# Kernel optimization log

Measured on AMD Instinct MI355X. Metric: run time of the kernel, lower is better.

## Reference

```python
import jax, jax.numpy as jnp
import numpy as np

REG_COEF = 25.0


def setup_inputs() -> dict:
    key = jax.random.key(0)
    k1, k2, k3, k4 = jax.random.split(key, 4)
    B, C, N, RES = 32, 4, 16384, 32
    y_pred = jax.random.normal(k1, (B, C, 4), dtype=jnp.float32)
    points = jax.random.uniform(k2, (B, N, 3), dtype=jnp.float32)  # unit cube
    voxel_grid = jax.random.uniform(k3, (B, RES, RES, RES), dtype=jnp.float32)
    voxel_grid_cp = jax.random.uniform(k4, (B, RES, RES, RES, 3), dtype=jnp.float32)
    return {"y_pred": y_pred, "points": points, "voxel_grid": voxel_grid,
            "voxel_grid_cp": voxel_grid_cp}


def _sym_loss(y_pred, points, voxel_grid, voxel_grid_cp):
    B, C, _ = y_pred.shape
    res = voxel_grid_cp.shape[1]
    normals = y_pred[:, :, 0:3]                       # [B,C,3]
    n_hat = normals / jnp.linalg.norm(normals, axis=-1, keepdims=True)
    d = y_pred[:, :, 3]                               # [B,C]

    # --- regularization loss: ||N N^T - I||_F per batch item, then mean ---
    gram = jnp.einsum('bcd,bed->bce', n_hat, n_hat) - jnp.eye(C, dtype=y_pred.dtype)
    reg_loss = jnp.linalg.norm(gram, axis=(1, 2))     # [B]

    # --- reflexion loss: reflect points across each plane, gather closest points ---
    # signed distance to plane: points . n_hat + d  -> [B,C,N]
    dist = jnp.einsum('bnd,bcd->bcn', points, n_hat) + d[:, :, None]
    reflected = points[:, None, :, :] - 2.0 * dist[..., None] * n_hat[:, :, None, :]  # [B,C,N,3]

    vox = jnp.clip(jnp.floor(reflected * res), 0, res - 1).astype(jnp.int32)  # [B,C,N,3]
    b_idx = jnp.arange(B)[:, None, None]
    cp = voxel_grid_cp[b_idx, vox[..., 0], vox[..., 1], vox[..., 2]]          # [B,C,N,3]

    per_plane = jnp.linalg.norm(reflected - cp, axis=-1).mean(axis=-1)        # [B,C]
    reflexion_loss = per_plane.sum()

    return jnp.reshape(reflexion_loss + REG_COEF * reg_loss.mean(), (1,))


def reference(y_pred, points, voxel_grid, voxel_grid_cp):
    return _sym_loss(y_pred, points, voxel_grid, voxel_grid_cp)
```

## Files before the change

### kernel.cpp

```cpp
#include <hip/hip_runtime.h>
#include <math.h>

#define B_    32
#define C_    4
#define N_    16384
#define RES_  32

#define CHUNKS 64
#define TPB    256

__global__ __launch_bounds__(TPB) void sym_main(
    const float* __restrict__ y_pred,
    const float* __restrict__ points,
    const float* __restrict__ cp,
    float* __restrict__ partials)
{
  const int id   = blockIdx.x;
  const int xcd  = id & 7;
  const int slot = id >> 3;
  const int b     = xcd + 8 * (slot & 3);
  const int chunk = slot >> 2;

  const float* yp = y_pred + b * (C_ * 4);
  float nx[C_], ny[C_], nz[C_], dd[C_];
#pragma unroll
  for (int c = 0; c < C_; ++c) {
    float ax = yp[c * 4 + 0];
    float ay = yp[c * 4 + 1];
    float az = yp[c * 4 + 2];
    float inv = 1.0f / sqrtf(ax * ax + ay * ay + az * az);
    nx[c] = ax * inv;
    ny[c] = ay * inv;
    nz[c] = az * inv;
    dd[c] = yp[c * 4 + 3];
  }

  const float* pb  = points + (size_t)b * (N_ * 3);
  const float* cpb = cp + (size_t)b * (RES_ * RES_ * RES_ * 3);

  const int p = chunk * TPB + threadIdx.x;
  const float px = pb[p * 3 + 0];
  const float py = pb[p * 3 + 1];
  const float pz = pb[p * 3 + 2];

  float rx[C_], ry[C_], rz[C_];
  int lin[C_];
#pragma unroll
  for (int c = 0; c < C_; ++c) {
    float dist = px * nx[c] + py * ny[c] + pz * nz[c] + dd[c];
    float t2 = 2.0f * dist;
    float x = px - t2 * nx[c];
    float y = py - t2 * ny[c];
    float z = pz - t2 * nz[c];
    rx[c] = x; ry[c] = y; rz[c] = z;
    int vx = (int)fminf(fmaxf(floorf(x * (float)RES_), 0.0f), (float)(RES_ - 1));
    int vy = (int)fminf(fmaxf(floorf(y * (float)RES_), 0.0f), (float)(RES_ - 1));
    int vz = (int)fminf(fmaxf(floorf(z * (float)RES_), 0.0f), (float)(RES_ - 1));
    lin[c] = ((vx * RES_ + vy) * RES_ + vz) * 3;
  }

  float cx[C_], cy[C_], cz[C_];
#pragma unroll
  for (int c = 0; c < C_; ++c) {
    cx[c] = cpb[lin[c] + 0];
    cy[c] = cpb[lin[c] + 1];
    cz[c] = cpb[lin[c] + 2];
  }

  float a0 = 0.0f, a1 = 0.0f;
#pragma unroll
  for (int c = 0; c < C_; c += 2) {
    float dx0 = rx[c+0] - cx[c+0], dy0 = ry[c+0] - cy[c+0], dz0 = rz[c+0] - cz[c+0];
    float dx1 = rx[c+1] - cx[c+1], dy1 = ry[c+1] - cy[c+1], dz1 = rz[c+1] - cz[c+1];
    a0 += sqrtf(dx0 * dx0 + dy0 * dy0 + dz0 * dz0);
    a1 += sqrtf(dx1 * dx1 + dy1 * dy1 + dz1 * dz1);
  }
  float acc = a0 + a1;

#pragma unroll
  for (int off = 32; off > 0; off >>= 1)
    acc += __shfl_down(acc, off, 64);

  __shared__ float sred[TPB / 64];
  const int lane = threadIdx.x & 63;
  const int wave = threadIdx.x >> 6;
  if (lane == 0) sred[wave] = acc;
  __syncthreads();
  if (threadIdx.x == 0) {
    float tot = 0.0f;
#pragma unroll
    for (int w = 0; w < TPB / 64; ++w) tot += sred[w];
    partials[b * CHUNKS + chunk] = tot;
  }
}

__global__ __launch_bounds__(256) void sym_final(
    const float* __restrict__ y_pred,
    const float* __restrict__ partials,
    float* __restrict__ out)
{
  __shared__ double sd[256];
  double acc = 0.0;
  for (int i = threadIdx.x; i < B_ * CHUNKS; i += 256)
    acc += (double)partials[i];
  acc *= (1.0 / (double)N_);

  if (threadIdx.x < B_) {
    const int b = threadIdx.x;
    const float* yp = y_pred + b * (C_ * 4);
    float nh[C_][3];
#pragma unroll
    for (int c = 0; c < C_; ++c) {
      float ax = yp[c * 4 + 0];
      float ay = yp[c * 4 + 1];
      float az = yp[c * 4 + 2];
      float inv = 1.0f / sqrtf(ax * ax + ay * ay + az * az);
      nh[c][0] = ax * inv;
      nh[c][1] = ay * inv;
      nh[c][2] = az * inv;
    }
    float s = 0.0f;
#pragma unroll
    for (int c = 0; c < C_; ++c) {
#pragma unroll
      for (int e = 0; e < C_; ++e) {
        float dot = nh[c][0] * nh[e][0] + nh[c][1] * nh[e][1] + nh[c][2] * nh[e][2];
        float g = dot - ((c == e) ? 1.0f : 0.0f);
        s += g * g;
      }
    }
    acc += (25.0 / (double)B_) * (double)sqrtf(s);
  }

  sd[threadIdx.x] = acc;
  __syncthreads();
  for (int off = 128; off > 0; off >>= 1) {
    if (threadIdx.x < off) sd[threadIdx.x] += sd[threadIdx.x + off];
    __syncthreads();
  }
  if (threadIdx.x == 0) out[0] = (float)sd[0];
}

extern "C" void kernel_launch(void* const* d_in, const int* in_sizes, int n_in,
                              void* d_out, int out_size, void* d_ws, size_t ws_size,
                              hipStream_t stream) {
  const float* y_pred = (const float*)d_in[0];
  const float* points = (const float*)d_in[1];
  const float* cp     = (const float*)d_in[3];
  float* partials = (float*)d_ws;
  float* out = (float*)d_out;

  sym_main<<<B_ * CHUNKS, TPB, 0, stream>>>(y_pred, points, cp, partials);
  sym_final<<<1, 256, 0, stream>>>(y_pred, partials, out);
}
```

Before: 82.30 us.

## Stage closest-point grid through LDS as fp16 quarters instead of random global gathers

Each block now handles 2048 points of one batch item with 1024 threads. It streams that batch item's closest-point grid into shared memory one quarter at a time, packed as three fp16 values per 64-bit word. Each reflected point then reads its closest point from LDS during the pass whose quarter holds its voxel. This replaces scattered global gathers with coalesced loads and LDS lookups. The trade-offs are that each block rereads the whole grid, which adds redundant traffic across the 8 chunks per batch item, and that fp16 storage loses precision. The loop over quarters also has divergent conditional accumulation.

```diff
diff --git a/kernel.cpp b/kernel.cpp
--- a/kernel.cpp
+++ b/kernel.cpp
@@ -1,13 +1,20 @@
 #include <hip/hip_runtime.h>
+#include <hip/hip_fp16.h>
 #include <math.h>
 
 #define B_    32
 #define C_    4
 #define N_    16384
 #define RES_  32
+#define VOX   (RES_ * RES_ * RES_)
 
-#define CHUNKS 64
-#define TPB    256
+#define TPB    1024
+#define CHUNKS 8
+#define GRID   (B_ * CHUNKS)
+#define PPB    (N_ / CHUNKS)
+#define PTS    (PPB / TPB)
+#define NG     (PTS * C_)
+#define QV     8192
 
 __global__ __launch_bounds__(TPB) void sym_main(
     const float* __restrict__ y_pred,
@@ -36,52 +43,75 @@
   }
 
   const float* pb  = points + (size_t)b * (N_ * 3);
-  const float* cpb = cp + (size_t)b * (RES_ * RES_ * RES_ * 3);
+  const float* cpb = cp + (size_t)b * (VOX * 3);
 
-  const int p = chunk * TPB + threadIdx.x;
-  const float px = pb[p * 3 + 0];
-  const float py = pb[p * 3 + 1];
-  const float pz = pb[p * 3 + 2];
-
-  float rx[C_], ry[C_], rz[C_];
-  int lin[C_];
+  float rx[NG], ry[NG], rz[NG];
+  int loc[NG], qr[NG];
 #pragma unroll
-  for (int c = 0; c < C_; ++c) {
-    float dist = px * nx[c] + py * ny[c] + pz * nz[c] + dd[c];
-    float t2 = 2.0f * dist;
-    float x = px - t2 * nx[c];
-    float y = py - t2 * ny[c];
-    float z = pz - t2 * nz[c];
-    rx[c] = x; ry[c] = y; rz[c] = z;
-    int vx = (int)fminf(fmaxf(floorf(x * (float)RES_), 0.0f), (float)(RES_ - 1));
-    int vy = (int)fminf(fmaxf(floorf(y * (float)RES_), 0.0f), (float)(RES_ - 1));
-    int vz = (int)fminf(fmaxf(floorf(z * (float)RES_), 0.0f), (float)(RES_ - 1));
-    lin[c] = ((vx * RES_ + vy) * RES_ + vz) * 3;
+  for (int k = 0; k < PTS; ++k) {
+    const int p = chunk * PPB + k * TPB + threadIdx.x;
+    const float px = pb[p * 3 + 0];
+    const float py = pb[p * 3 + 1];
+    const float pz = pb[p * 3 + 2];
+#pragma unroll
+    for (int c = 0; c < C_; ++c) {
+      const int g = k * C_ + c;
+      float dist = px * nx[c] + py * ny[c] + pz * nz[c] + dd[c];
+      float t2 = 2.0f * dist;
+      float x = px - t2 * nx[c];
+      float y = py - t2 * ny[c];
+      float z = pz - t2 * nz[c];
+      rx[g] = x; ry[g] = y; rz[g] = z;
+      int vx = (int)fminf(fmaxf(floorf(x * (float)RES_), 0.0f), (float)(RES_ - 1));
+      int vy = (int)fminf(fmaxf(floorf(y * (float)RES_), 0.0f), (float)(RES_ - 1));
+      int vz = (int)fminf(fmaxf(floorf(z * (float)RES_), 0.0f), (float)(RES_ - 1));
+      int lin = (vx * RES_ + vy) * RES_ + vz;
+      qr[g]  = lin >> 13;
+      loc[g] = lin & (QV - 1);
+    }
   }
 
-  float cx[C_], cy[C_], cz[C_];
+  __shared__ unsigned long long tab[QV];
+  float acc = 0.0f;
+
+  for (int q = 0; q < 4; ++q) {
+    if (q) __syncthreads();
+    const float* src = cpb + (size_t)q * QV * 3;
 #pragma unroll
-  for (int c = 0; c < C_; ++c) {
-    cx[c] = cpb[lin[c] + 0];
-    cy[c] = cpb[lin[c] + 1];
-    cz[c] = cpb[lin[c] + 2];
+    for (int i = 0; i < QV / TPB; ++i) {
+      const int v = i * TPB + threadIdx.x;
+      float x = src[v * 3 + 0];
+      float y = src[v * 3 + 1];
+      float z = src[v * 3 + 2];
+      unsigned long long w =
+          (unsigned long long)__half_as_ushort(__float2half(x)) |
+          ((unsigned long long)__half_as_ushort(__float2half(y)) << 16) |
+          ((unsigned long long)__half_as_ushort(__float2half(z)) << 32);
+      tab[v] = w;
+    }
+    __syncthreads();
+
+#pragma unroll
+    for (int g = 0; g < NG; ++g) {
+      if (qr[g] == q) {
+        unsigned long long w = tab[loc[g]];
+        float fx = __half2float(__ushort_as_half((unsigned short)(w)));
+        float fy = __half2float(__ushort_as_half((unsigned short)(w >> 16)));
+        float fz = __half2float(__ushort_as_half((unsigned short)(w >> 32)));
+        float dx = rx[g] - fx;
+        float dy = ry[g] - fy;
+        float dz = rz[g] - fz;
+        acc += sqrtf(dx * dx + dy * dy + dz * dz);
+      }
+    }
   }
-
-  float a0 = 0.0f, a1 = 0.0f;
-#pragma unroll
-  for (int c = 0; c < C_; c += 2) {
-    float dx0 = rx[c+0] - cx[c+0], dy0 = ry[c+0] - cy[c+0], dz0 = rz[c+0] - cz[c+0];
-    float dx1 = rx[c+1] - cx[c+1], dy1 = ry[c+1] - cy[c+1], dz1 = rz[c+1] - cz[c+1];
-    a0 += sqrtf(dx0 * dx0 + dy0 * dy0 + dz0 * dz0);
-    a1 += sqrtf(dx1 * dx1 + dy1 * dy1 + dz1 * dz1);
-  }
-  float acc = a0 + a1;
 
 #pragma unroll
   for (int off = 32; off > 0; off >>= 1)
     acc += __shfl_down(acc, off, 64);
 
-  __shared__ float sred[TPB / 64];
+  __syncthreads();
+  float* sred = (float*)tab;
   const int lane = threadIdx.x & 63;
   const int wave = threadIdx.x >> 6;
   if (lane == 0) sred[wave] = acc;
@@ -101,7 +131,7 @@
 {
   __shared__ double sd[256];
   double acc = 0.0;
-  for (int i = threadIdx.x; i < B_ * CHUNKS; i += 256)
+  for (int i = threadIdx.x; i < GRID; i += 256)
     acc += (double)partials[i];
   acc *= (1.0 / (double)N_);
 
@@ -150,6 +180,6 @@
   float* partials = (float*)d_ws;
   float* out = (float*)d_out;
 
-  sym_main<<<B_ * CHUNKS, TPB, 0, stream>>>(y_pred, points, cp, partials);
-  sym_final<<<1, 256, 0, stream>>>(y_pred, partials, out);
+  sym_main <<<GRID, TPB, 0, stream>>>(y_pred, points, cp, partials);
+  sym_final<<<1,    256, 0, stream>>>(y_pred, partials, out);
 }
```

Measured after the change: 85.75 us. 4.2% more time.
